# Performance work log

Measured on AMD Instinct MI355X. Metric: run time of the kernel, lower is better.

Reference implementation:

```python
import jax, jax.numpy as jnp
import numpy as np

B, L, C, OUT = 8, 256, 512, 512


def setup_inputs() -> dict:
    key = jax.random.key(0)
    ks = jax.random.split(key, 8)
    xd = jax.random.normal(ks[0], (B, L, C), jnp.float32)
    xt = jax.random.normal(ks[1], (B, L, C), jnp.float32)
    # Linear weights stored (in, out): y = x @ W + b (equiv. to torch x @ W^T)
    Wc = jax.random.normal(ks[2], (C, C), jnp.float32) * 0.02
    bc = jnp.zeros((C,), jnp.float32)
    Wp = jax.random.normal(ks[3], (C, C), jnp.float32) * 0.02
    bp = jnp.zeros((C,), jnp.float32)
    Wf = jax.random.normal(ks[4], (C, OUT), jnp.float32) * 0.02
    bf = jnp.zeros((OUT,), jnp.float32)
    return {"xd": xd, "xt": xt, "Wc": Wc, "bc": bc, "Wp": Wp, "bp": bp, "Wf": Wf, "bf": bf}


def reference(xd, xt, Wc, bc, Wp, bp, Wf, bf):
    # projected features
    pt = jax.nn.relu(xt) @ Wp + bp              # (b, Lt, C)
    pc = jax.nn.relu(xd) @ Wc + bc              # (b, Ld, C)
    # sigmoid bilinear scores: (b, Lt, Ld) == (b, Ld, Lt) since Lt == Ld structurally
    scores = jax.nn.sigmoid(jnp.einsum('bic,bkc->bik', pt, pc))
    # normalize by total per-batch sum
    w = scores / jnp.sum(scores, axis=(1, 2), keepdims=True)
    # tanh of elementwise outer product, reduced with attention weights
    # cp[b,c] = sum_{i,j} tanh(xd[b,i,c] * xt[b,j,c]) * w[b,i,j]
    cp = jnp.einsum('bijc,bij->bc', jnp.tanh(xd[:, :, None, :] * xt[:, None, :, :]), w)
    return cp @ Wf + bf
```

## Files before the change

### kernel.cpp

```cpp
#include <hip/hip_runtime.h>
#include <math.h>

#define B_   8
#define L_   256
#define C_   512
#define OUT_ 512

typedef _Float16 half8 __attribute__((ext_vector_type(8)));
typedef _Float16 half4 __attribute__((ext_vector_type(4)));
typedef float    f32x4 __attribute__((ext_vector_type(4)));
typedef float    f32x2 __attribute__((ext_vector_type(2)));

__global__ __launch_bounds__(256)
void proj_mfma_kernel(const float* __restrict__ xt, const float* __restrict__ Wp,
                      const float* __restrict__ bp,
                      const float* __restrict__ xd, const float* __restrict__ Wc,
                      const float* __restrict__ bc,
                      _Float16* __restrict__ pt, _Float16* __restrict__ pc)
{
    const int which = blockIdx.z;
    const float* __restrict__ X    = which ? xd : xt;
    const float* __restrict__ W    = which ? Wc : Wp;
    const float* __restrict__ bias = which ? bc : bp;
    _Float16*    __restrict__ Y    = which ? pc : pt;

    __shared__ _Float16 Ah[2][32][40];
    __shared__ _Float16 Bh[2][64][40];
    __shared__ _Float16 Ot[32][72];

    const int tid = threadIdx.x;
    const int m0 = blockIdx.y << 5, n0 = blockIdx.x << 6;
    const int lane = tid & 63, wv = tid >> 6;
    const int l15 = lane & 15, quad = lane >> 4;
    const int mblk = wv & 1, npair = wv >> 1;

    const int srow = tid >> 2, sch = (tid & 3) << 3;
    const float* Ag = X + (size_t)(m0 + (srow & 31)) * C_ + sch;
    const int nl = tid & 63, kseg = tid >> 6;
    const float* Bg = W + (size_t)(kseg << 3) * C_ + n0 + nl;

    float4 a0 = {}, a1 = {};
    if (tid < 128) { a0 = *(const float4*)(Ag); a1 = *(const float4*)(Ag + 4); }
    float wr[8];
    #pragma unroll
    for (int r = 0; r < 8; ++r) wr[r] = Bg[(size_t)r * C_];

    if (tid < 128) {
        half8 av;
        av[0] = (_Float16)fmaxf(a0.x, 0.f); av[1] = (_Float16)fmaxf(a0.y, 0.f);
        av[2] = (_Float16)fmaxf(a0.z, 0.f); av[3] = (_Float16)fmaxf(a0.w, 0.f);
        av[4] = (_Float16)fmaxf(a1.x, 0.f); av[5] = (_Float16)fmaxf(a1.y, 0.f);
        av[6] = (_Float16)fmaxf(a1.z, 0.f); av[7] = (_Float16)fmaxf(a1.w, 0.f);
        *(half8*)&Ah[0][srow][sch] = av;
    }
    {
        half8 bv;
        #pragma unroll
        for (int r = 0; r < 8; ++r) bv[r] = (_Float16)wr[r];
        *(half8*)&Bh[0][nl][kseg << 3] = bv;
    }

    f32x4 acc[2] = {};
    for (int ks = 0; ks < 16; ++ks) {
        const int cur = ks & 1;
        if (ks < 15) {
            Bg += 32 * C_;
            if (tid < 128) {
                Ag += 32;
                a0 = *(const float4*)(Ag);
                a1 = *(const float4*)(Ag + 4);
            }
            #pragma unroll
            for (int r = 0; r < 8; ++r) wr[r] = Bg[(size_t)r * C_];
        }
        __syncthreads();
        half8 af = *(const half8*)&Ah[cur][(mblk << 4) + l15][quad << 3];
        #pragma unroll
        for (int nb = 0; nb < 2; ++nb) {
            half8 bf = *(const half8*)&Bh[cur][(npair << 5) + (nb << 4) + l15][quad << 3];
            acc[nb] = __builtin_amdgcn_mfma_f32_16x16x32_f16(af, bf, acc[nb], 0, 0, 0);
        }
        if (ks < 15) {
            if (tid < 128) {
                half8 av;
                av[0] = (_Float16)fmaxf(a0.x, 0.f); av[1] = (_Float16)fmaxf(a0.y, 0.f);
                av[2] = (_Float16)fmaxf(a0.z, 0.f); av[3] = (_Float16)fmaxf(a0.w, 0.f);
                av[4] = (_Float16)fmaxf(a1.x, 0.f); av[5] = (_Float16)fmaxf(a1.y, 0.f);
                av[6] = (_Float16)fmaxf(a1.z, 0.f); av[7] = (_Float16)fmaxf(a1.w, 0.f);
                *(half8*)&Ah[cur ^ 1][srow][sch] = av;
            }
            half8 bv;
            #pragma unroll
            for (int r = 0; r < 8; ++r) bv[r] = (_Float16)wr[r];
            *(half8*)&Bh[cur ^ 1][nl][kseg << 3] = bv;
        }
    }

    __syncthreads();
    #pragma unroll
    for (int nb = 0; nb < 2; ++nb) {
        const int n = (npair << 5) + (nb << 4) + l15;
        const float bz = bias[n0 + n];
        #pragma unroll
        for (int r = 0; r < 4; ++r)
            Ot[(mblk << 4) + (quad << 2) + r][n] = (_Float16)(acc[nb][r] + bz);
    }
    __syncthreads();
    const int erow = tid >> 3, ech = (tid & 7) << 3;
    *(half8*)&Y[(size_t)(m0 + erow) * C_ + n0 + ech] = *(const half8*)&Ot[erow][ech];
}

__device__ __forceinline__ float sigmoid_fast(float z) {
    float e = __builtin_amdgcn_exp2f(-1.4426950408889634f * z);
    return __builtin_amdgcn_rcpf(e + 1.0f);
}

__global__ __launch_bounds__(256, 6)
void cp_scores_kernel(const _Float16* __restrict__ pt, const _Float16* __restrict__ pc,
                      const float* __restrict__ xd, const float* __restrict__ xt,
                      float* __restrict__ partials, float* __restrict__ sums_part)
{
    const int bx = blockIdx.x, by = blockIdx.y;
    const int b = blockIdx.z >> 1, ch = blockIdx.z & 1;
    const int i0 = bx << 5, j0 = by << 4;
    const int tid = threadIdx.x;
    const int lane = tid & 63, wv = tid >> 6;
    const int l15 = lane & 15, quad = lane >> 4;

    __shared__ _Float16 Ah[2][32][40];
    __shared__ _Float16 Bh[2][16][40];
    __shared__ float ws_[16][36];
    __shared__ float wred[2];

    const int srow = tid >> 2;
    const int sch  = (tid & 3) << 3;
    const _Float16* Sg = ((srow < 32) ? pt + (size_t)(b * L_ + i0 + srow) * C_
                                      : pc + (size_t)(b * L_ + j0 + (srow - 32)) * C_) + sch;

    half8 v = {};
    if (tid < 192) v = *(const half8*)Sg;
    if (tid < 192) {
        if (srow < 32) *(half8*)&Ah[0][srow][sch] = v;
        else           *(half8*)&Bh[0][srow - 32][sch] = v;
    }

    f32x4 acc = {};
    for (int ks = 0; ks < 16; ++ks) {
        const int cur = ks & 1;
        if (ks < 15 && tid < 192) { Sg += 32; v = *(const half8*)Sg; }
        __syncthreads();
        if (wv < 2) {
            half8 af = *(const half8*)&Ah[cur][(wv << 4) + l15][quad << 3];
            half8 bf = *(const half8*)&Bh[cur][l15][quad << 3];
            acc = __builtin_amdgcn_mfma_f32_16x16x32_f16(af, bf, acc, 0, 0, 0);
        }
        if (ks < 15 && tid < 192) {
            if (srow < 32) *(half8*)&Ah[cur ^ 1][srow][sch] = v;
            else           *(half8*)&Bh[cur ^ 1][srow - 32][sch] = v;
        }
    }

    float lsum = 0.f;
    if (wv < 2) {
        float4 sg;
        sg.x = sigmoid_fast(acc[0]);
        sg.y = sigmoid_fast(acc[1]);
        sg.z = sigmoid_fast(acc[2]);
        sg.w = sigmoid_fast(acc[3]);
        *(float4*)&ws_[l15][(wv << 4) + (quad << 2)] = sg;
        lsum = (sg.x + sg.y) + (sg.z + sg.w);
    }
    #pragma unroll
    for (int off = 32; off; off >>= 1) lsum += __shfl_xor(lsum, off);
    if (wv < 2 && lane == 0) wred[wv] = lsum;
    __syncthreads();
    if (tid == 0 && ch == 0)
        sums_part[(b << 7) | (bx << 4) | by] = wred[0] + wred[1];

    const int c = (ch << 8) | tid;
    const float* __restrict__ xdb = xd + (size_t)(b * L_ + i0) * C_ + c;
    const float* __restrict__ xtb = xt + (size_t)(b * L_ + j0) * C_ + c;
    f32x2 xds2[16];
    #pragma unroll
    for (int i = 0; i < 16; ++i) {
        xds2[i].x = xdb[(size_t)(2 * i) * C_]     * 2.8853900817779268f;
        xds2[i].y = xdb[(size_t)(2 * i + 1) * C_] * 2.8853900817779268f;
    }

    f32x2 acc01 = {0.f, 0.f}, acc23 = {0.f, 0.f};
    #pragma unroll 4
    for (int jj = 0; jj < 16; ++jj) {
        const float xv = xtb[(size_t)jj * C_];
        #pragma unroll
        for (int i = 0; i < 32; i += 4) {
            const float4 w4 = *(const float4*)&ws_[jj][i];
            f32x2 x01 = xds2[i >> 1] * xv;
            f32x2 e01 = { __builtin_amdgcn_exp2f(x01.x), __builtin_amdgcn_exp2f(x01.y) };
            f32x2 q01 = e01 + 1.0f;
            float rp01 = __builtin_amdgcn_rcpf(q01.x * q01.y);
            f32x2 r01 = rp01 * __builtin_shufflevector(q01, q01, 1, 0);
            f32x2 w01 = { w4.x, w4.y };
            acc01 = w01 * r01 + acc01;
            f32x2 x23 = xds2[(i >> 1) + 1] * xv;
            f32x2 e23 = { __builtin_amdgcn_exp2f(x23.x), __builtin_amdgcn_exp2f(x23.y) };
            f32x2 q23 = e23 + 1.0f;
            float rp23 = __builtin_amdgcn_rcpf(q23.x * q23.y);
            f32x2 r23 = rp23 * __builtin_shufflevector(q23, q23, 1, 0);
            f32x2 w23 = { w4.z, w4.w };
            acc23 = w23 * r23 + acc23;
        }
    }
    const int p = (bx << 4) | by;
    partials[(size_t)((b << 7) | p) * C_ + c] =
        (acc01.x + acc01.y) + (acc23.x + acc23.y);
}

__global__ __launch_bounds__(512)
void finalize_kernel(const float* __restrict__ partials, const float* __restrict__ sums_part,
                     const float* __restrict__ Wf, const float* __restrict__ bfv,
                     float* __restrict__ out)
{
    const int b = blockIdx.y;
    const int t = threadIdx.x;
    __shared__ float cp[C_];
    __shared__ float red[512];
    __shared__ float sumsh;

    red[t] = (t < 128) ? sums_part[(b << 7) | t] : 0.f;

    float s = 0.f;
    #pragma unroll
    for (int p = 0; p < 128; ++p)
        s += partials[(size_t)((b << 7) | p) * C_ + t];

    __syncthreads();
    for (int st = 256; st > 0; st >>= 1) {
        if (t < st) red[t] += red[t + st];
        __syncthreads();
    }
    if (t == 0) sumsh = red[0];
    __syncthreads();

    cp[t] = 1.0f - 2.0f * s / sumsh;
    __syncthreads();

    const int o  = ((int)blockIdx.x << 6) | (t & 63);
    const int c0 = (t >> 6) << 6;
    float acc = 0.f;
    #pragma unroll 8
    for (int i = 0; i < 64; ++i) {
        const int cc = c0 + i;
        acc = fmaf(cp[cc], Wf[(size_t)cc * OUT_ + o], acc);
    }
    red[t] = acc;
    __syncthreads();
    if (t < 64) {
        float a = 0.f;
        #pragma unroll
        for (int g = 0; g < 8; ++g) a += red[(g << 6) | t];
        out[(size_t)b * OUT_ + o] = a + bfv[o];
    }
}

extern "C" void kernel_launch(void* const* d_in, const int* in_sizes, int n_in,
                              void* d_out, int out_size, void* d_ws, size_t ws_size,
                              hipStream_t stream)
{
    const float* xd = (const float*)d_in[0];
    const float* xt = (const float*)d_in[1];
    const float* Wc = (const float*)d_in[2];
    const float* bc = (const float*)d_in[3];
    const float* Wp = (const float*)d_in[4];
    const float* bp = (const float*)d_in[5];
    const float* Wf = (const float*)d_in[6];
    const float* bf = (const float*)d_in[7];
    float* out = (float*)d_out;

    _Float16* pt  = (_Float16*)d_ws;
    _Float16* pc  = pt + 1048576;
    float* partials  = (float*)(pc + 1048576);
    float* sums_part = partials + B_ * 128 * C_;

    proj_mfma_kernel<<<dim3(8, 64, 2), 256, 0, stream>>>(xt, Wp, bp, xd, Wc, bc, pt, pc);
    cp_scores_kernel<<<dim3(8, 16, 16), 256, 0, stream>>>(pt, pc, xd, xt, partials, sums_part);
    finalize_kernel<<<dim3(8, 8), 512, 0, stream>>>(partials, sums_part, Wf, bf, out);
}
```

Measured before the change: 143.8 us.

## Enlarge projection tiles, merge channel halves, reduce partials via atomics

The projection GEMM tile grows from 32 to 64 rows so every thread loads A and each wave computes four MFMA tiles. The cp_scores kernel now uses 512-thread blocks covering all channels, so the score MFMA and sigmoid are no longer recomputed per channel half. Per-tile partial sums are accumulated with atomicAdd into a small per-batch buffer that is zeroed by a memset, replacing the large partials array and the 128-way reduction in finalize. This trades partials traffic for atomic contention and makes summation order nondeterministic.

```diff
diff --git a/kernel.cpp b/kernel.cpp
--- a/kernel.cpp
+++ b/kernel.cpp
@@ -7,7 +7,6 @@
 #define OUT_ 512
 
 typedef _Float16 half8 __attribute__((ext_vector_type(8)));
-typedef _Float16 half4 __attribute__((ext_vector_type(4)));
 typedef float    f32x4 __attribute__((ext_vector_type(4)));
 typedef float    f32x2 __attribute__((ext_vector_type(2)));
 
@@ -24,71 +23,64 @@
     const float* __restrict__ bias = which ? bc : bp;
     _Float16*    __restrict__ Y    = which ? pc : pt;
 
-    __shared__ _Float16 Ah[2][32][40];
+    __shared__ _Float16 Ah[2][64][40];
     __shared__ _Float16 Bh[2][64][40];
-    __shared__ _Float16 Ot[32][72];
+    __shared__ _Float16 Ot[64][72];
 
     const int tid = threadIdx.x;
-    const int m0 = blockIdx.y << 5, n0 = blockIdx.x << 6;
+    const int m0 = blockIdx.y << 6, n0 = blockIdx.x << 6;
     const int lane = tid & 63, wv = tid >> 6;
     const int l15 = lane & 15, quad = lane >> 4;
-    const int mblk = wv & 1, npair = wv >> 1;
 
     const int srow = tid >> 2, sch = (tid & 3) << 3;
-    const float* Ag = X + (size_t)(m0 + (srow & 31)) * C_ + sch;
+    const float* Ag = X + (size_t)(m0 + srow) * C_ + sch;
     const int nl = tid & 63, kseg = tid >> 6;
     const float* Bg = W + (size_t)(kseg << 3) * C_ + n0 + nl;
 
-    float4 a0 = {}, a1 = {};
-    if (tid < 128) { a0 = *(const float4*)(Ag); a1 = *(const float4*)(Ag + 4); }
+    float4 a0 = *(const float4*)(Ag);
+    float4 a1 = *(const float4*)(Ag + 4);
     float wr[8];
     #pragma unroll
     for (int r = 0; r < 8; ++r) wr[r] = Bg[(size_t)r * C_];
 
-    if (tid < 128) {
+    {
         half8 av;
         av[0] = (_Float16)fmaxf(a0.x, 0.f); av[1] = (_Float16)fmaxf(a0.y, 0.f);
         av[2] = (_Float16)fmaxf(a0.z, 0.f); av[3] = (_Float16)fmaxf(a0.w, 0.f);
         av[4] = (_Float16)fmaxf(a1.x, 0.f); av[5] = (_Float16)fmaxf(a1.y, 0.f);
         av[6] = (_Float16)fmaxf(a1.z, 0.f); av[7] = (_Float16)fmaxf(a1.w, 0.f);
         *(half8*)&Ah[0][srow][sch] = av;
-    }
-    {
         half8 bv;
         #pragma unroll
         for (int r = 0; r < 8; ++r) bv[r] = (_Float16)wr[r];
         *(half8*)&Bh[0][nl][kseg << 3] = bv;
     }
 
-    f32x4 acc[2] = {};
+    f32x4 acc[4] = {};
     for (int ks = 0; ks < 16; ++ks) {
         const int cur = ks & 1;
         if (ks < 15) {
+            Ag += 32;
             Bg += 32 * C_;
-            if (tid < 128) {
-                Ag += 32;
-                a0 = *(const float4*)(Ag);
-                a1 = *(const float4*)(Ag + 4);
-            }
+            a0 = *(const float4*)(Ag);
+            a1 = *(const float4*)(Ag + 4);
             #pragma unroll
             for (int r = 0; r < 8; ++r) wr[r] = Bg[(size_t)r * C_];
         }
         __syncthreads();
-        half8 af = *(const half8*)&Ah[cur][(mblk << 4) + l15][quad << 3];
-        #pragma unroll
-        for (int nb = 0; nb < 2; ++nb) {
-            half8 bf = *(const half8*)&Bh[cur][(npair << 5) + (nb << 4) + l15][quad << 3];
+        half8 af = *(const half8*)&Ah[cur][(wv << 4) + l15][quad << 3];
+        #pragma unroll
+        for (int nb = 0; nb < 4; ++nb) {
+            half8 bf = *(const half8*)&Bh[cur][(nb << 4) + l15][quad << 3];
             acc[nb] = __builtin_amdgcn_mfma_f32_16x16x32_f16(af, bf, acc[nb], 0, 0, 0);
         }
         if (ks < 15) {
-            if (tid < 128) {
-                half8 av;
-                av[0] = (_Float16)fmaxf(a0.x, 0.f); av[1] = (_Float16)fmaxf(a0.y, 0.f);
-                av[2] = (_Float16)fmaxf(a0.z, 0.f); av[3] = (_Float16)fmaxf(a0.w, 0.f);
-                av[4] = (_Float16)fmaxf(a1.x, 0.f); av[5] = (_Float16)fmaxf(a1.y, 0.f);
-                av[6] = (_Float16)fmaxf(a1.z, 0.f); av[7] = (_Float16)fmaxf(a1.w, 0.f);
-                *(half8*)&Ah[cur ^ 1][srow][sch] = av;
-            }
+            half8 av;
+            av[0] = (_Float16)fmaxf(a0.x, 0.f); av[1] = (_Float16)fmaxf(a0.y, 0.f);
+            av[2] = (_Float16)fmaxf(a0.z, 0.f); av[3] = (_Float16)fmaxf(a0.w, 0.f);
+            av[4] = (_Float16)fmaxf(a1.x, 0.f); av[5] = (_Float16)fmaxf(a1.y, 0.f);
+            av[6] = (_Float16)fmaxf(a1.z, 0.f); av[7] = (_Float16)fmaxf(a1.w, 0.f);
+            *(half8*)&Ah[cur ^ 1][srow][sch] = av;
             half8 bv;
             #pragma unroll
             for (int r = 0; r < 8; ++r) bv[r] = (_Float16)wr[r];
@@ -98,16 +90,17 @@
 
     __syncthreads();
     #pragma unroll
-    for (int nb = 0; nb < 2; ++nb) {
-        const int n = (npair << 5) + (nb << 4) + l15;
-        const float bz = bias[n0 + n];
+    for (int nb = 0; nb < 4; ++nb) {
+        const float bz = bias[n0 + (nb << 4) + l15];
         #pragma unroll
         for (int r = 0; r < 4; ++r)
-            Ot[(mblk << 4) + (quad << 2) + r][n] = (_Float16)(acc[nb][r] + bz);
+            Ot[(wv << 4) + (quad << 2) + r][(nb << 4) + l15] = (_Float16)(acc[nb][r] + bz);
     }
     __syncthreads();
     const int erow = tid >> 3, ech = (tid & 7) << 3;
-    *(half8*)&Y[(size_t)(m0 + erow) * C_ + n0 + ech] = *(const half8*)&Ot[erow][ech];
+    #pragma unroll
+    for (int h = 0; h < 64; h += 32)
+        *(half8*)&Y[(size_t)(m0 + erow + h) * C_ + n0 + ech] = *(const half8*)&Ot[erow + h][ech];
 }
 
 __device__ __forceinline__ float sigmoid_fast(float z) {
@@ -115,13 +108,12 @@
     return __builtin_amdgcn_rcpf(e + 1.0f);
 }
 
-__global__ __launch_bounds__(256, 6)
+__global__ __launch_bounds__(512, 4)
 void cp_scores_kernel(const _Float16* __restrict__ pt, const _Float16* __restrict__ pc,
                       const float* __restrict__ xd, const float* __restrict__ xt,
-                      float* __restrict__ partials, float* __restrict__ sums_part)
-{
-    const int bx = blockIdx.x, by = blockIdx.y;
-    const int b = blockIdx.z >> 1, ch = blockIdx.z & 1;
+                      float* __restrict__ P, float* __restrict__ sums_part)
+{
+    const int bx = blockIdx.x, by = blockIdx.y, b = blockIdx.z;
     const int i0 = bx << 5, j0 = by << 4;
     const int tid = threadIdx.x;
     const int lane = tid & 63, wv = tid >> 6;
@@ -138,8 +130,8 @@
                                       : pc + (size_t)(b * L_ + j0 + (srow - 32)) * C_) + sch;
 
     half8 v = {};
-    if (tid < 192) v = *(const half8*)Sg;
     if (tid < 192) {
+        v = *(const half8*)Sg;
         if (srow < 32) *(half8*)&Ah[0][srow][sch] = v;
         else           *(half8*)&Bh[0][srow - 32][sch] = v;
     }
@@ -174,10 +166,10 @@
     for (int off = 32; off; off >>= 1) lsum += __shfl_xor(lsum, off);
     if (wv < 2 && lane == 0) wred[wv] = lsum;
     __syncthreads();
-    if (tid == 0 && ch == 0)
+    if (tid == 0)
         sums_part[(b << 7) | (bx << 4) | by] = wred[0] + wred[1];
 
-    const int c = (ch << 8) | tid;
+    const int c = tid;
     const float* __restrict__ xdb = xd + (size_t)(b * L_ + i0) * C_ + c;
     const float* __restrict__ xtb = xt + (size_t)(b * L_ + j0) * C_ + c;
     f32x2 xds2[16];
@@ -210,54 +202,46 @@
             acc23 = w23 * r23 + acc23;
         }
     }
-    const int p = (bx << 4) | by;
-    partials[(size_t)((b << 7) | p) * C_ + c] =
-        (acc01.x + acc01.y) + (acc23.x + acc23.y);
-}
-
-__global__ __launch_bounds__(512)
-void finalize_kernel(const float* __restrict__ partials, const float* __restrict__ sums_part,
+    atomicAdd(&P[(b << 9) | c], (acc01.x + acc01.y) + (acc23.x + acc23.y));
+}
+
+__global__ __launch_bounds__(256)
+void finalize_kernel(const float* __restrict__ P, const float* __restrict__ sums_part,
                      const float* __restrict__ Wf, const float* __restrict__ bfv,
                      float* __restrict__ out)
 {
     const int b = blockIdx.y;
     const int t = threadIdx.x;
     __shared__ float cp[C_];
-    __shared__ float red[512];
+    __shared__ float red[256];
     __shared__ float sumsh;
 
     red[t] = (t < 128) ? sums_part[(b << 7) | t] : 0.f;
-
-    float s = 0.f;
-    #pragma unroll
-    for (int p = 0; p < 128; ++p)
-        s += partials[(size_t)((b << 7) | p) * C_ + t];
-
-    __syncthreads();
-    for (int st = 256; st > 0; st >>= 1) {
-        if (t < st) red[t] += red[t + st];
+    __syncthreads();
+    for (int st = 64; st > 0; st >>= 1) {
+        if (t < st) red[t] += red[t + st] + ((st == 64) ? red[t + 128] : 0.f);
         __syncthreads();
     }
     if (t == 0) sumsh = red[0];
     __syncthreads();
 
-    cp[t] = 1.0f - 2.0f * s / sumsh;
-    __syncthreads();
-
-    const int o  = ((int)blockIdx.x << 6) | (t & 63);
-    const int c0 = (t >> 6) << 6;
+    const float inv = 2.0f / sumsh;
+    cp[t]       = 1.0f - P[(b << 9) | t] * inv;
+    cp[t + 256] = 1.0f - P[(b << 9) | (t + 256)] * inv;
+    __syncthreads();
+
+    const int o    = ((int)blockIdx.x << 6) | (t & 63);
+    const int cbase = (t >> 6) << 7;
     float acc = 0.f;
     #pragma unroll 8
-    for (int i = 0; i < 64; ++i) {
-        const int cc = c0 + i;
+    for (int i = 0; i < 128; ++i) {
+        const int cc = cbase + i;
         acc = fmaf(cp[cc], Wf[(size_t)cc * OUT_ + o], acc);
     }
     red[t] = acc;
     __syncthreads();
     if (t < 64) {
-        float a = 0.f;
-        #pragma unroll
-        for (int g = 0; g < 8; ++g) a += red[(g << 6) | t];
+        float a = ((red[t] + red[t + 64]) + (red[t + 128] + red[t + 192]));
         out[(size_t)b * OUT_ + o] = a + bfv[o];
     }
 }
@@ -278,10 +262,11 @@
 
     _Float16* pt  = (_Float16*)d_ws;
     _Float16* pc  = pt + 1048576;
-    float* partials  = (float*)(pc + 1048576);
-    float* sums_part = partials + B_ * 128 * C_;
-
-    proj_mfma_kernel<<<dim3(8, 64, 2), 256, 0, stream>>>(xt, Wp, bp, xd, Wc, bc, pt, pc);
-    cp_scores_kernel<<<dim3(8, 16, 16), 256, 0, stream>>>(pt, pc, xd, xt, partials, sums_part);
-    finalize_kernel<<<dim3(8, 8), 512, 0, stream>>>(partials, sums_part, Wf, bf, out);
-}
+    float* P         = (float*)(pc + 1048576);
+    float* sums_part = P + B_ * C_;
+
+    hipMemsetAsync(P, 0, B_ * C_ * sizeof(float), stream);
+    proj_mfma_kernel<<<dim3(8, 32, 2), 256, 0, stream>>>(xt, Wp, bp, xd, Wc, bc, pt, pc);
+    cp_scores_kernel<<<dim3(8, 16, 8), 512, 0, stream>>>(pt, pc, xd, xt, P, sums_part);
+    finalize_kernel<<<dim3(8, 8), 256, 0, stream>>>(P, sums_part, Wf, bf, out);
+}
```

After: 142.2 us. About the same (-1.1%).
